# Kernel tuning notes

Hardware: AMD Instinct MI355X
Metric: run time of the kernel (lower is better)

## Reference

```python
import jax, jax.numpy as jnp
import numpy as np


def setup_inputs() -> dict:
    key = jax.random.key(0)
    k1, k2, k3, k4 = jax.random.split(key, 4)
    B, T, C, H = 8, 2048, 1024, 1024
    return {
        "x": jax.random.normal(k1, (B, T, C), dtype=jnp.float32),
        "Wk": jax.random.normal(k2, (H, C), dtype=jnp.float32),
        "Wq": jax.random.normal(k3, (H, C), dtype=jnp.float32),
        "Wv": jax.random.normal(k4, (H, C), dtype=jnp.float32),
    }


def reference(x, Wk, Wq, Wv):
    # x: [B, T, C]; Wk/Wq/Wv: [H, C] (torch Linear stores [fan_out, fan_in])
    B, T, C = x.shape
    k = jnp.einsum('btc,hc->bth', x, Wk)  # [B, T, H]
    q = jnp.einsum('btc,hc->bth', x, Wq)
    v = jnp.einsum('btc,hc->bth', x, Wv)
    # NOTE: source scales by n_embd (C) ** -0.5, not head_size
    wei = jnp.einsum('bth,bsh->bts', q, k) * (C ** -0.5)  # [B, T, T]
    causal = jnp.tril(jnp.ones((T, T), dtype=bool))
    wei = jnp.where(causal, wei, -jnp.inf)
    wei = jax.nn.softmax(wei, axis=-1)
    # Dropout omitted (inference behavior; p=0.5 train-only in source)
    out = jnp.einsum('bts,bsh->bth', wei, v)  # [B, T, H]
    return (out, wei)
```

## Files before the change

### kernel.cpp

```cpp
#include <hip/hip_runtime.h>
#include <hip/hip_bf16.h>


#define BB 8
#define TT 2048
#define CC 1024
#define HH 1024
#define BT (BB * TT)

typedef _Float16 f16x8 __attribute__((ext_vector_type(8)));
typedef _Float16 f16x4 __attribute__((ext_vector_type(4)));
typedef float f32x4 __attribute__((ext_vector_type(4)));

#define AS1 __attribute__((address_space(1)))
#define AS3 __attribute__((address_space(3)))

__device__ __forceinline__ void gld16(const _Float16* g, _Float16* lds) {
    __builtin_amdgcn_global_load_lds((AS1 const unsigned int*)g,
                                     (AS3 unsigned int*)lds, 16, 0, 0);
}

__global__ __launch_bounds__(256) void split_kernel(
    const float* __restrict__ src, _Float16* __restrict__ dh,
    _Float16* __restrict__ dl, int n)
{
    int i = (blockIdx.x * 256 + threadIdx.x) * 4;
    if (i >= n) return;
    float4 v = *(const float4*)(src + i);
    f16x4 h, l;
    h[0] = (_Float16)v.x; l[0] = (_Float16)(v.x - (float)h[0]);
    h[1] = (_Float16)v.y; l[1] = (_Float16)(v.y - (float)h[1]);
    h[2] = (_Float16)v.z; l[2] = (_Float16)(v.z - (float)h[2]);
    h[3] = (_Float16)v.w; l[3] = (_Float16)(v.w - (float)h[3]);
    *(f16x4*)&dh[i] = h;
    *(f16x4*)&dl[i] = l;
}

__global__ __launch_bounds__(256) void splitT_kernel(
    const float* __restrict__ W, _Float16* __restrict__ th,
    _Float16* __restrict__ tl)
{
    __shared__ float L[64][65];
    const int h0 = blockIdx.x * 64;
    const int c0 = blockIdx.y * 64;
    const int tid = threadIdx.x;
    {
        const int hl = tid >> 2;
        const int cs = (tid & 3) * 16;
#pragma unroll
        for (int jj = 0; jj < 16; jj += 4) {
            float4 v = *(const float4*)&W[(size_t)(h0 + hl) * CC + c0 + cs + jj];
            L[cs + jj + 0][hl] = v.x;
            L[cs + jj + 1][hl] = v.y;
            L[cs + jj + 2][hl] = v.z;
            L[cs + jj + 3][hl] = v.w;
        }
    }
    __syncthreads();
    const int c  = tid >> 2;
    const int hs = (tid & 3) * 16;
    f16x8 hv0, hv1, lv0, lv1;
#pragma unroll
    for (int i = 0; i < 8; ++i) {
        float a = L[c][hs + i], b = L[c][hs + 8 + i];
        hv0[i] = (_Float16)a; lv0[i] = (_Float16)(a - (float)hv0[i]);
        hv1[i] = (_Float16)b; lv1[i] = (_Float16)(b - (float)hv1[i]);
    }
    size_t o = (size_t)(c0 + c) * HH + h0 + hs;
    *(f16x8*)&th[o] = hv0; *(f16x8*)&th[o + 8] = hv1;
    *(f16x8*)&tl[o] = lv0; *(f16x8*)&tl[o + 8] = lv1;
}

__global__ __launch_bounds__(256, 2) void mm_kernel(
    const _Float16* __restrict__ aH, const _Float16* __restrict__ aL,
    const _Float16* __restrict__ bH, const _Float16* __restrict__ bL,
    _Float16* __restrict__ mtH, _Float16* __restrict__ mtL)
{
    __shared__ _Float16 Ah[4096], Al[4096], Bh[4096], Bl[4096];

    const int n0 = blockIdx.x * 128;
    const int m0 = blockIdx.y * 128;

    const int tid  = threadIdx.x;
    const int r0   = tid & 127;
    const int k0   = tid >> 7;
    const int wave = tid >> 6;
    const int lane = tid & 63;
    const int quad = lane >> 4;
    const int lrow = lane & 15;
    const int wr   = (wave >> 1) * 64;
    const int wc   = (wave & 1) * 64;

    const size_t ga = (size_t)(m0 + r0) * HH + k0 * 8;
    const size_t gb = (size_t)(n0 + r0) * HH + k0 * 8;
    const int lds0 = tid * 8, lds1 = (tid + 256) * 8;

    f32x4 acc[4][4] = {};

    for (int kc = 0; kc < HH; kc += 32) {
        __syncthreads();
        gld16(aH + ga + kc,      &Ah[lds0]);
        gld16(aH + ga + kc + 16, &Ah[lds1]);
        gld16(aL + ga + kc,      &Al[lds0]);
        gld16(aL + ga + kc + 16, &Al[lds1]);
        gld16(bH + gb + kc,      &Bh[lds0]);
        gld16(bH + gb + kc + 16, &Bh[lds1]);
        gld16(bL + gb + kc,      &Bl[lds0]);
        gld16(bL + gb + kc + 16, &Bl[lds1]);
        __syncthreads();

        f16x8 ahf[4], alf[4], bhf[4], blf[4];
#pragma unroll
        for (int i = 0; i < 4; ++i) {
            ahf[i] = *(const f16x8*)&Ah[(quad * 128 + wr + i * 16 + lrow) * 8];
            alf[i] = *(const f16x8*)&Al[(quad * 128 + wr + i * 16 + lrow) * 8];
            bhf[i] = *(const f16x8*)&Bh[(quad * 128 + wc + i * 16 + lrow) * 8];
            blf[i] = *(const f16x8*)&Bl[(quad * 128 + wc + i * 16 + lrow) * 8];
        }
#pragma unroll
        for (int i = 0; i < 4; ++i)
#pragma unroll
            for (int j = 0; j < 4; ++j) {
                acc[i][j] = __builtin_amdgcn_mfma_f32_16x16x32_f16(ahf[i], bhf[j], acc[i][j], 0, 0, 0);
                acc[i][j] = __builtin_amdgcn_mfma_f32_16x16x32_f16(ahf[i], blf[j], acc[i][j], 0, 0, 0);
                acc[i][j] = __builtin_amdgcn_mfma_f32_16x16x32_f16(alf[i], bhf[j], acc[i][j], 0, 0, 0);
            }
    }

#pragma unroll
    for (int i = 0; i < 4; ++i)
#pragma unroll
        for (int j = 0; j < 4; ++j) {
            int mm = m0 + wr + i * 16 + quad * 4;
            int nn = n0 + wc + j * 16 + lrow;
            f16x4 ph, pl;
#pragma unroll
            for (int r = 0; r < 4; ++r) {
                float val = acc[i][j][r];
                _Float16 h = (_Float16)val;
                ph[r] = h;
                pl[r] = (_Float16)(val - (float)h);
            }
            *(f16x4*)&mtH[(size_t)nn * CC + mm] = ph;
            *(f16x4*)&mtL[(size_t)nn * CC + mm] = pl;
        }
}

#define EPI_STRIDE 136
__global__ __launch_bounds__(256, 2) void pv_kernel(
    const _Float16* __restrict__ xh, const _Float16* __restrict__ xl,
    const _Float16* __restrict__ mtH, const _Float16* __restrict__ mtL,
    const _Float16* __restrict__ Wvh,
    _Float16* __restrict__ Ph, _Float16* __restrict__ Pl,
    _Float16* __restrict__ vT)
{
    __shared__ _Float16 S[40960];

    const int idx   = blockIdx.x;
    const int z     = idx >> 10;
    const int r     = idx & 1023;
    const int xcd   = r & 7;
    const int j7    = r >> 3;
    const int mtile = xcd * 16 + (j7 >> 3);
    const int ntile = j7 & 7;
    const int m0 = mtile * 128;
    const int n0 = ntile * 128;

    const int tid  = threadIdx.x;
    const int r0   = tid & 127;
    const int k0   = tid >> 7;
    const int wave = tid >> 6;
    const int lane = tid & 63;
    const int quad = lane >> 4;
    const int lrow = lane & 15;
    const int wr   = (wave >> 1) * 64;
    const int wc   = (wave & 1) * 64;

    const size_t ga = (size_t)(m0 + r0) * CC + k0 * 8;
    const size_t gb = (size_t)(n0 + r0) * CC + k0 * 8;
    const int lds0 = tid * 8, lds1 = (tid + 256) * 8;

    f32x4 acc[4][4] = {};

    if (z == 0) {
#define PV_A(kc_, sp_) do { \
        _Float16* Sb = S + (sp_) * 8192; \
        gld16(xh + ga + (kc_),      &Sb[lds0]); \
        gld16(xh + ga + (kc_) + 16, &Sb[lds1]); \
        gld16(xl + ga + (kc_),      &Sb[4096 + lds0]); \
        gld16(xl + ga + (kc_) + 16, &Sb[4096 + lds1]); \
    } while (0)
#define PV_B(kc_, sp_) do { \
        _Float16* Sb = S + 24576 + (sp_) * 8192; \
        gld16(mtH + gb + (kc_),      &Sb[lds0]); \
        gld16(mtH + gb + (kc_) + 16, &Sb[lds1]); \
        gld16(mtL + gb + (kc_),      &Sb[4096 + lds0]); \
        gld16(mtL + gb + (kc_) + 16, &Sb[4096 + lds1]); \
    } while (0)
        PV_A(0, 0);
        PV_B(0, 0);
        PV_A(32, 1);
        int sa = 0, sb = 0;
        for (int kc = 0; kc < CC; kc += 32) {
            asm volatile("s_waitcnt vmcnt(4)" ::: "memory");
            __builtin_amdgcn_s_barrier();
            __builtin_amdgcn_sched_barrier(0);

            int kb = kc + 32; if (kb > CC - 32) kb = CC - 32;
            PV_B(kb, sb ^ 1);
            int ka = kc + 64; if (ka > CC - 32) ka = CC - 32;
            int s2 = sa + 2; if (s2 >= 3) s2 -= 3;
            PV_A(ka, s2);

            const _Float16* Ah = S + sa * 8192;
            const _Float16* Al = Ah + 4096;
            const _Float16* Bh = S + 24576 + sb * 8192;
            const _Float16* Bl = Bh + 4096;

            f16x8 ahf[4], alf[4], bhf[4], blf[4];
#pragma unroll
            for (int i = 0; i < 4; ++i) {
                ahf[i] = *(const f16x8*)&Ah[(quad * 128 + wr + i * 16 + lrow) * 8];
                alf[i] = *(const f16x8*)&Al[(quad * 128 + wr + i * 16 + lrow) * 8];
                bhf[i] = *(const f16x8*)&Bh[(quad * 128 + wc + i * 16 + lrow) * 8];
                blf[i] = *(const f16x8*)&Bl[(quad * 128 + wc + i * 16 + lrow) * 8];
            }
#pragma unroll
            for (int i = 0; i < 4; ++i)
#pragma unroll
                for (int j = 0; j < 4; ++j) {
                    acc[i][j] = __builtin_amdgcn_mfma_f32_16x16x32_f16(ahf[i], bhf[j], acc[i][j], 0, 0, 0);
                    acc[i][j] = __builtin_amdgcn_mfma_f32_16x16x32_f16(ahf[i], blf[j], acc[i][j], 0, 0, 0);
                    acc[i][j] = __builtin_amdgcn_mfma_f32_16x16x32_f16(alf[i], bhf[j], acc[i][j], 0, 0, 0);
                }

            ++sa; if (sa == 3) sa = 0;
            sb ^= 1;
        }
    } else {
#define PV_S1(kc_, sp_) do { \
        _Float16* Sb = S + (sp_) * 8192; \
        gld16(xh  + ga + (kc_),      &Sb[lds0]); \
        gld16(xh  + ga + (kc_) + 16, &Sb[lds1]); \
        gld16(Wvh + gb + (kc_),      &Sb[4096 + lds0]); \
        gld16(Wvh + gb + (kc_) + 16, &Sb[4096 + lds1]); \
    } while (0)
        PV_S1(0, 0);
        PV_S1(32, 1);
        int sl = 0;
        for (int kc = 0; kc < CC; kc += 32) {
            asm volatile("s_waitcnt vmcnt(4)" ::: "memory");
            __builtin_amdgcn_s_barrier();
            __builtin_amdgcn_sched_barrier(0);

            int kpre = kc + 64;
            if (kpre > CC - 32) kpre = CC - 32;
            int s2 = sl + 2; if (s2 >= 3) s2 -= 3;
            PV_S1(kpre, s2);

            const _Float16* Ah = S + sl * 8192;
            const _Float16* Bh = Ah + 4096;

            f16x8 ahf[4], bhf[4];
#pragma unroll
            for (int i = 0; i < 4; ++i) {
                ahf[i] = *(const f16x8*)&Ah[(quad * 128 + wr + i * 16 + lrow) * 8];
                bhf[i] = *(const f16x8*)&Bh[(quad * 128 + wc + i * 16 + lrow) * 8];
            }
#pragma unroll
            for (int i = 0; i < 4; ++i)
#pragma unroll
                for (int j = 0; j < 4; ++j)
                    acc[i][j] = __builtin_amdgcn_mfma_f32_16x16x32_f16(ahf[i], bhf[j], acc[i][j], 0, 0, 0);

            ++sl; if (sl == 3) sl = 0;
        }
    }

    asm volatile("s_waitcnt vmcnt(0)" ::: "memory");
    __syncthreads();

    if (z == 1) {
#pragma unroll
        for (int i = 0; i < 4; ++i)
#pragma unroll
            for (int j = 0; j < 4; ++j) {
                int hl = wc + j * 16 + lrow;
                int tl = wr + i * 16 + quad * 4;
                f16x4 p;
#pragma unroll
                for (int rr = 0; rr < 4; ++rr) p[rr] = (_Float16)acc[i][j][rr];
                *(f16x4*)&S[hl * EPI_STRIDE + tl] = p;
            }
        __syncthreads();
        const int bi  = mtile >> 4;
        const int t0g = (mtile & 15) * 128;
        _Float16* vb = vT + (size_t)bi * HH * TT;
#pragma unroll
        for (int rr = 0; rr < 128; rr += 16) {
            int h = rr + (tid >> 4);
            int t = (tid & 15) * 8;
            f16x8 val = *(const f16x8*)&S[h * EPI_STRIDE + t];
            *(f16x8*)&vb[(size_t)(n0 + h) * TT + t0g + t] = val;
        }
    } else {
#pragma unroll
        for (int i = 0; i < 4; ++i)
#pragma unroll
            for (int j = 0; j < 4; ++j) {
                int tl = wr + i * 16 + quad * 4;
                int cl = wc + j * 16 + lrow;
#pragma unroll
                for (int rr = 0; rr < 4; ++rr)
                    S[(tl + rr) * EPI_STRIDE + cl] = (_Float16)acc[i][j][rr];
            }
        __syncthreads();
#pragma unroll
        for (int rr = 0; rr < 128; rr += 16) {
            int t = rr + (tid >> 4);
            int c = (tid & 15) * 8;
            f16x8 val = *(const f16x8*)&S[t * EPI_STRIDE + c];
            *(f16x8*)&Ph[(size_t)(m0 + t) * CC + n0 + c] = val;
        }
        __syncthreads();
#pragma unroll
        for (int i = 0; i < 4; ++i)
#pragma unroll
            for (int j = 0; j < 4; ++j) {
                int tl = wr + i * 16 + quad * 4;
                int cl = wc + j * 16 + lrow;
#pragma unroll
                for (int rr = 0; rr < 4; ++rr) {
                    float val = acc[i][j][rr];
                    _Float16 h = (_Float16)val;
                    S[(tl + rr) * EPI_STRIDE + cl] = (_Float16)(val - (float)h);
                }
            }
        __syncthreads();
#pragma unroll
        for (int rr = 0; rr < 128; rr += 16) {
            int t = rr + (tid >> 4);
            int c = (tid & 15) * 8;
            f16x8 val = *(const f16x8*)&S[t * EPI_STRIDE + c];
            *(f16x8*)&Pl[(size_t)(m0 + t) * CC + n0 + c] = val;
        }
    }
}

__global__ __launch_bounds__(256, 2) void logits_kernel(
    const _Float16* __restrict__ Ph, const _Float16* __restrict__ Pl,
    const _Float16* __restrict__ xh, const _Float16* __restrict__ xl,
    float* __restrict__ wei)
{
    __shared__ _Float16 S[40960];

    const int id  = blockIdx.x;
    const int b   = id & 7;
    const int tri = id >> 3;
    int tt = (int)((sqrtf(8.0f * (float)tri + 1.0f) - 1.0f) * 0.5f);
    while ((tt + 1) * (tt + 2) / 2 <= tri) ++tt;
    while (tt * (tt + 1) / 2 > tri) --tt;
    const int st = tri - tt * (tt + 1) / 2;

    const size_t base = (size_t)b * TT * CC;
    float* wb = wei + (size_t)b * TT * TT;
    const int m0 = tt * 128;
    const int n0 = st * 128;

    const int tid  = threadIdx.x;
    const int r0   = tid & 127;
    const int k0   = tid >> 7;
    const int wave = tid >> 6;
    const int lane = tid & 63;
    const int quad = lane >> 4;
    const int lrow = lane & 15;
    const int wr   = (wave >> 1) * 64;
    const int wc   = (wave & 1) * 64;

    const size_t ga = base + (size_t)(m0 + r0) * CC + k0 * 8;
    const size_t gb = base + (size_t)(n0 + r0) * CC + k0 * 8;
    const int lds0 = tid * 8, lds1 = (tid + 256) * 8;

    f32x4 acc[4][4] = {};

#define LG_A(kc_, sp_) do { \
    _Float16* Sb = S + (sp_) * 8192; \
    gld16(Ph + ga + (kc_),      &Sb[lds0]); \
    gld16(Ph + ga + (kc_) + 16, &Sb[lds1]); \
    gld16(Pl + ga + (kc_),      &Sb[4096 + lds0]); \
    gld16(Pl + ga + (kc_) + 16, &Sb[4096 + lds1]); \
} while (0)
#define LG_B(kc_, sp_) do { \
    _Float16* Sb = S + 24576 + (sp_) * 8192; \
    gld16(xh + gb + (kc_),      &Sb[lds0]); \
    gld16(xh + gb + (kc_) + 16, &Sb[lds1]); \
    gld16(xl + gb + (kc_),      &Sb[4096 + lds0]); \
    gld16(xl + gb + (kc_) + 16, &Sb[4096 + lds1]); \
} while (0)

    LG_A(0, 0);
    LG_B(0, 0);
    LG_A(32, 1);

    int sa = 0, sb = 0;
    for (int kc = 0; kc < CC; kc += 32) {
        asm volatile("s_waitcnt vmcnt(4)" ::: "memory");
        __builtin_amdgcn_s_barrier();
        __builtin_amdgcn_sched_barrier(0);

        int kb = kc + 32; if (kb > CC - 32) kb = CC - 32;
        LG_B(kb, sb ^ 1);
        int ka = kc + 64; if (ka > CC - 32) ka = CC - 32;
        int s2 = sa + 2; if (s2 >= 3) s2 -= 3;
        LG_A(ka, s2);

        const _Float16* Ah = S + sa * 8192;
        const _Float16* Al = Ah + 4096;
        const _Float16* Bh = S + 24576 + sb * 8192;
        const _Float16* Bl = Bh + 4096;

        f16x8 ahf[4], alf[4], bhf[4], blf[4];
#pragma unroll
        for (int i = 0; i < 4; ++i) {
            ahf[i] = *(const f16x8*)&Ah[(quad * 128 + wr + i * 16 + lrow) * 8];
            alf[i] = *(const f16x8*)&Al[(quad * 128 + wr + i * 16 + lrow) * 8];
            bhf[i] = *(const f16x8*)&Bh[(quad * 128 + wc + i * 16 + lrow) * 8];
            blf[i] = *(const f16x8*)&Bl[(quad * 128 + wc + i * 16 + lrow) * 8];
        }
#pragma unroll
        for (int i = 0; i < 4; ++i)
#pragma unroll
            for (int j = 0; j < 4; ++j) {
                acc[i][j] = __builtin_amdgcn_mfma_f32_16x16x32_f16(ahf[i], bhf[j], acc[i][j], 0, 0, 0);
                acc[i][j] = __builtin_amdgcn_mfma_f32_16x16x32_f16(ahf[i], blf[j], acc[i][j], 0, 0, 0);
                acc[i][j] = __builtin_amdgcn_mfma_f32_16x16x32_f16(alf[i], bhf[j], acc[i][j], 0, 0, 0);
            }

        ++sa; if (sa == 3) sa = 0;
        sb ^= 1;
    }

    asm volatile("s_waitcnt vmcnt(0)" ::: "memory");

    const float scale = 0.03125f;
#pragma unroll
    for (int i = 0; i < 4; ++i)
#pragma unroll
        for (int j = 0; j < 4; ++j)
#pragma unroll
            for (int r = 0; r < 4; ++r) {
                int rr = wr + i * 16 + quad * 4 + r;
                int cc = wc + j * 16 + lrow;
                wb[(size_t)(m0 + rr) * TT + n0 + cc] = acc[i][j][r] * scale;
            }
}

__global__ __launch_bounds__(256) void softmax_kernel(
    float* __restrict__ wei, _Float16* __restrict__ wei16)
{
    const int t = blockIdx.x;
    const int b = blockIdx.y;
    float* row = wei + (size_t)b * TT * TT + (size_t)t * TT;
    _Float16* row16 = wei16 + (size_t)b * TT * TT + (size_t)t * TT;
    const int n = t + 1;
    const int tid = threadIdx.x;
    const int base = tid * 8;

    float vals[8];
    if (base < n) {
        float4 v0 = *(const float4*)&row[base];
        float4 v1 = *(const float4*)&row[base + 4];
        vals[0] = v0.x; vals[1] = v0.y; vals[2] = v0.z; vals[3] = v0.w;
        vals[4] = v1.x; vals[5] = v1.y; vals[6] = v1.z; vals[7] = v1.w;
    } else {
#pragma unroll
        for (int i = 0; i < 8; ++i) vals[i] = -INFINITY;
    }

    float mx = -INFINITY;
#pragma unroll
    for (int i = 0; i < 8; ++i) {
        if (base + i >= n) vals[i] = -INFINITY;
        mx = fmaxf(mx, vals[i]);
    }
#pragma unroll
    for (int off = 32; off > 0; off >>= 1)
        mx = fmaxf(mx, __shfl_down(mx, off));

    __shared__ float redm[4];
    __shared__ float reds[4];
    if ((tid & 63) == 0) redm[tid >> 6] = mx;
    __syncthreads();
    const float m = fmaxf(fmaxf(redm[0], redm[1]), fmaxf(redm[2], redm[3]));

    float sum = 0.f;
#pragma unroll
    for (int i = 0; i < 8; ++i) {
        vals[i] = __expf(vals[i] - m);
        sum += vals[i];
    }
#pragma unroll
    for (int off = 32; off > 0; off >>= 1)
        sum += __shfl_down(sum, off);
    if ((tid & 63) == 0) reds[tid >> 6] = sum;
    __syncthreads();
    const float inv = 1.0f / (reds[0] + reds[1] + reds[2] + reds[3]);

    f16x8 h;
#pragma unroll
    for (int i = 0; i < 8; ++i) {
        float w = vals[i] * inv;
        vals[i] = w;
        h[i] = (_Float16)w;
    }
    *(float4*)&row[base]     = make_float4(vals[0], vals[1], vals[2], vals[3]);
    *(float4*)&row[base + 4] = make_float4(vals[4], vals[5], vals[6], vals[7]);
    *(f16x8*)&row16[base]    = h;
}

__global__ __launch_bounds__(256, 3) void out_kernel(
    const _Float16* __restrict__ wei16, const _Float16* __restrict__ vT,
    float* __restrict__ out)
{
    __shared__ _Float16 S[24576];

    const int id = blockIdx.x;
    const int b  = id & 7;
    const int r  = id >> 3;
    const int tt = 15 - (r >> 3);
    const int nb = r & 7;

    const _Float16* wb = wei16 + (size_t)b * TT * TT;
    const _Float16* vb = vT    + (size_t)b * HH * TT;
    float*          ob = out   + (size_t)b * TT * HH;

    const int m0 = tt * 128;
    const int n0 = nb * 128;
    const int kend = (tt + 1) * 128;

    const int tid  = threadIdx.x;
    const int r0   = tid & 127;
    const int k0   = tid >> 7;
    const int wave = tid >> 6;
    const int lane = tid & 63;
    const int quad = lane >> 4;
    const int lrow = lane & 15;
    const int wr   = (wave >> 1) * 64;
    const int wc   = (wave & 1) * 64;

    const size_t ga = (size_t)(m0 + r0) * TT + k0 * 8;
    const size_t gb = (size_t)(n0 + r0) * TT + k0 * 8;
    const int lds0 = tid * 8, lds1 = (tid + 256) * 8;

    f32x4 acc[4][4] = {};

#define OUT_STAGE(kc_, sp_) do { \
    _Float16* Sb = S + (sp_) * 8192; \
    gld16(wb + ga + (kc_),      &Sb[lds0]); \
    gld16(wb + ga + (kc_) + 16, &Sb[lds1]); \
    gld16(vb + gb + (kc_),      &Sb[4096 + lds0]); \
    gld16(vb + gb + (kc_) + 16, &Sb[4096 + lds1]); \
} while (0)

    OUT_STAGE(0, 0);
    OUT_STAGE(32, 1);

    int sl = 0;
    for (int kc = 0; kc < kend; kc += 32) {
        asm volatile("s_waitcnt vmcnt(4)" ::: "memory");
        __builtin_amdgcn_s_barrier();
        __builtin_amdgcn_sched_barrier(0);

        int kpre = kc + 64;
        if (kpre > kend - 32) kpre = kend - 32;
        int s2 = sl + 2; if (s2 >= 3) s2 -= 3;
        OUT_STAGE(kpre, s2);

        const _Float16* Ah = S + sl * 8192;
        const _Float16* Bh = Ah + 4096;

        f16x8 ahf[4], bhf[4];
#pragma unroll
        for (int i = 0; i < 4; ++i) {
            ahf[i] = *(const f16x8*)&Ah[(quad * 128 + wr + i * 16 + lrow) * 8];
            bhf[i] = *(const f16x8*)&Bh[(quad * 128 + wc + i * 16 + lrow) * 8];
        }
#pragma unroll
        for (int i = 0; i < 4; ++i)
#pragma unroll
            for (int j = 0; j < 4; ++j)
                acc[i][j] = __builtin_amdgcn_mfma_f32_16x16x32_f16(ahf[i], bhf[j], acc[i][j], 0, 0, 0);

        ++sl; if (sl == 3) sl = 0;
    }

    asm volatile("s_waitcnt vmcnt(0)" ::: "memory");

#pragma unroll
    for (int i = 0; i < 4; ++i)
#pragma unroll
        for (int j = 0; j < 4; ++j)
#pragma unroll
            for (int r2 = 0; r2 < 4; ++r2) {
                int rr = wr + i * 16 + quad * 4 + r2;
                int cc = wc + j * 16 + lrow;
                ob[(size_t)(m0 + rr) * HH + n0 + cc] = acc[i][j][r2];
            }
}

extern "C" void kernel_launch(void* const* d_in, const int* in_sizes, int n_in,
                              void* d_out, int out_size, void* d_ws, size_t ws_size,
                              hipStream_t stream)
{
    const float* x  = (const float*)d_in[0];
    const float* Wk = (const float*)d_in[1];
    const float* Wq = (const float*)d_in[2];
    const float* Wv = (const float*)d_in[3];

    const size_t NX = (size_t)BT * CC;
    const size_t NW = (size_t)HH * CC;

    float* out = (float*)d_out;
    float* wei = out + (size_t)BT * HH;

    _Float16* WqTh = (_Float16*)out;
    _Float16* WqTl = WqTh + NW;
    _Float16* WkTh = WqTl + NW;
    _Float16* WkTl = WkTh + NW;
    _Float16* Wvh  = WkTl + NW;
    _Float16* Wvl  = Wvh  + NW;
    _Float16* MTh  = Wvl  + NW;
    _Float16* MTl  = MTh  + NW;

    _Float16* xh = (_Float16*)d_ws;
    _Float16* xl = xh + NX;
    _Float16* Ph = xl + NX;
    _Float16* Pl = Ph + NX;
    _Float16* vT = Pl + NX;
    _Float16* wei16 = (_Float16*)d_ws;

    split_kernel<<<dim3(NX / 1024), 256, 0, stream>>>(x, xh, xl, (int)NX);
    splitT_kernel<<<dim3(HH / 64, CC / 64), 256, 0, stream>>>(Wq, WqTh, WqTl);
    splitT_kernel<<<dim3(HH / 64, CC / 64), 256, 0, stream>>>(Wk, WkTh, WkTl);
    split_kernel<<<dim3(NW / 1024), 256, 0, stream>>>(Wv, Wvh, Wvl, (int)NW);

    mm_kernel<<<dim3(CC / 128, CC / 128), 256, 0, stream>>>(
        WqTh, WqTl, WkTh, WkTl, MTh, MTl);
    pv_kernel<<<dim3(2048), 256, 0, stream>>>(
        xh, xl, MTh, MTl, Wvh, Ph, Pl, vT);
    logits_kernel<<<dim3(136 * BB), 256, 0, stream>>>(
        Ph, Pl, xh, xl, wei);
    softmax_kernel<<<dim3(TT, BB), 256, 0, stream>>>(wei, wei16);
    out_kernel<<<dim3(128 * BB), 256, 0, stream>>>(wei16, vT, out);
}
```

Baseline: 797.9 us.

## Enlarge pv and off-diagonal logits tiles to 256x256 with 512-thread blocks

Rewrites pv_kernel and the off-diagonal part of the logits GEMM to use 256x256 output tiles, 512-thread blocks and a simple double-buffered LDS pipeline. Diagonal logits tiles move to a separate kernel that keeps 128x128 tiles. The larger tiles raise arithmetic intensity and cut global/L2 traffic per FLOP. In exchange there is higher register pressure (8x4 accumulators), 128KB of LDS per block, fewer blocks for load balancing, and the older finer-grained vmcnt pipelining is dropped.

Measured after the change: 843.8 us. 1.06x slower.

```diff
diff --git a/kernel.cpp b/kernel.cpp
--- a/kernel.cpp
+++ b/kernel.cpp
@@ -146,25 +146,284 @@
         }
 }
 
-#define EPI_STRIDE 136
-__global__ __launch_bounds__(256, 2) void pv_kernel(
+__global__ __launch_bounds__(512, 2) void pv_kernel(
     const _Float16* __restrict__ xh, const _Float16* __restrict__ xl,
     const _Float16* __restrict__ mtH, const _Float16* __restrict__ mtL,
     const _Float16* __restrict__ Wvh,
     _Float16* __restrict__ Ph, _Float16* __restrict__ Pl,
     _Float16* __restrict__ vT)
 {
+    __shared__ _Float16 S[65536];
+
+    const int id = blockIdx.x;
+    const int z  = id & 1;
+    const int q  = id >> 1;
+    const int xcd = q & 7;
+    const int s   = q >> 3;
+    const int mtile = xcd * 8 + (s >> 2);
+    const int ntile = s & 3;
+    const int m0 = mtile * 256;
+    const int n0 = ntile * 256;
+
+    const int tid  = threadIdx.x;
+    const int wave = tid >> 6;
+    const int lane = tid & 63;
+    const int quad = lane >> 4;
+    const int lrow = lane & 15;
+    const int mw   = wave >> 2;
+    const int nw   = wave & 3;
+
+    const size_t ga = (size_t)(m0 + (tid & 255)) * CC + (tid >> 8) * 8;
+    const size_t gb = (size_t)(n0 + (tid & 255)) * CC + (tid >> 8) * 8;
+    const int lds0 = tid * 8, lds1 = (tid + 512) * 8;
+
+    f32x4 acc[8][4] = {};
+
+    if (z == 0) {
+#define ST0(kc_, buf_) do { \
+        _Float16* Sb = S + (buf_) * 32768; \
+        gld16(xh  + ga + (kc_),      &Sb[lds0]); \
+        gld16(xh  + ga + (kc_) + 16, &Sb[lds1]); \
+        gld16(xl  + ga + (kc_),      &Sb[8192 + lds0]); \
+        gld16(xl  + ga + (kc_) + 16, &Sb[8192 + lds1]); \
+        gld16(mtH + gb + (kc_),      &Sb[16384 + lds0]); \
+        gld16(mtH + gb + (kc_) + 16, &Sb[16384 + lds1]); \
+        gld16(mtL + gb + (kc_),      &Sb[24576 + lds0]); \
+        gld16(mtL + gb + (kc_) + 16, &Sb[24576 + lds1]); \
+    } while (0)
+        ST0(0, 0);
+        int cur = 0;
+        for (int kc = 0; kc < CC; kc += 32) {
+            __syncthreads();
+            if (kc + 32 < CC) ST0(kc + 32, cur ^ 1);
+
+            const _Float16* Ab = S + cur * 32768;
+            const _Float16* Al_ = Ab + 8192;
+            const _Float16* Bb = Ab + 16384;
+            const _Float16* Bl_ = Ab + 24576;
+
+            f16x8 bh[4], bl[4];
+#pragma unroll
+            for (int j = 0; j < 4; ++j) {
+                int c = (quad * 256 + nw * 64 + j * 16 + lrow) * 8;
+                bh[j] = *(const f16x8*)&Bb[c];
+                bl[j] = *(const f16x8*)&Bl_[c];
+            }
+#pragma unroll
+            for (int i = 0; i < 8; ++i) {
+                int a = (quad * 256 + mw * 128 + i * 16 + lrow) * 8;
+                f16x8 ah = *(const f16x8*)&Ab[a];
+                f16x8 al = *(const f16x8*)&Al_[a];
+#pragma unroll
+                for (int j = 0; j < 4; ++j) {
+                    acc[i][j] = __builtin_amdgcn_mfma_f32_16x16x32_f16(ah, bh[j], acc[i][j], 0, 0, 0);
+                    acc[i][j] = __builtin_amdgcn_mfma_f32_16x16x32_f16(ah, bl[j], acc[i][j], 0, 0, 0);
+                    acc[i][j] = __builtin_amdgcn_mfma_f32_16x16x32_f16(al, bh[j], acc[i][j], 0, 0, 0);
+                }
+            }
+            cur ^= 1;
+        }
+
+#pragma unroll
+        for (int stream = 0; stream < 2; ++stream) {
+            _Float16* dst = stream ? Pl : Ph;
+#pragma unroll
+            for (int h = 0; h < 2; ++h) {
+                __syncthreads();
+                if (mw == h) {
+#pragma unroll
+                    for (int i = 0; i < 8; ++i)
+#pragma unroll
+                        for (int j = 0; j < 4; ++j)
+#pragma unroll
+                            for (int rr = 0; rr < 4; ++rr) {
+                                float v = acc[i][j][rr];
+                                _Float16 hi = (_Float16)v;
+                                _Float16 e = stream ? (_Float16)(v - (float)hi) : hi;
+                                S[(i * 16 + quad * 4 + rr) * 264 + nw * 64 + j * 16 + lrow] = e;
+                            }
+                }
+                __syncthreads();
+#pragma unroll
+                for (int w = 0; w < 8; ++w) {
+                    int x = w * 512 + tid;
+                    int row = x >> 5;
+                    int c8 = (x & 31) * 8;
+                    *(f16x8*)&dst[(size_t)(m0 + h * 128 + row) * CC + n0 + c8] =
+                        *(const f16x8*)&S[row * 264 + c8];
+                }
+            }
+        }
+    } else {
+#define ST1(kc_, buf_) do { \
+        _Float16* Sb = S + (buf_) * 16384; \
+        gld16(xh  + ga + (kc_),      &Sb[lds0]); \
+        gld16(xh  + ga + (kc_) + 16, &Sb[lds1]); \
+        gld16(Wvh + gb + (kc_),      &Sb[8192 + lds0]); \
+        gld16(Wvh + gb + (kc_) + 16, &Sb[8192 + lds1]); \
+    } while (0)
+        ST1(0, 0);
+        int cur = 0;
+        for (int kc = 0; kc < CC; kc += 32) {
+            __syncthreads();
+            if (kc + 32 < CC) ST1(kc + 32, cur ^ 1);
+
+            const _Float16* Ab = S + cur * 16384;
+            const _Float16* Bb = Ab + 8192;
+
+            f16x8 bh[4];
+#pragma unroll
+            for (int j = 0; j < 4; ++j)
+                bh[j] = *(const f16x8*)&Bb[(quad * 256 + nw * 64 + j * 16 + lrow) * 8];
+#pragma unroll
+            for (int i = 0; i < 8; ++i) {
+                f16x8 ah = *(const f16x8*)&Ab[(quad * 256 + mw * 128 + i * 16 + lrow) * 8];
+#pragma unroll
+                for (int j = 0; j < 4; ++j)
+                    acc[i][j] = __builtin_amdgcn_mfma_f32_16x16x32_f16(ah, bh[j], acc[i][j], 0, 0, 0);
+            }
+            cur ^= 1;
+        }
+
+        const int bi  = mtile >> 3;
+        const int t0g = (mtile & 7) * 256;
+        _Float16* vb = vT + (size_t)bi * HH * TT;
+#pragma unroll
+        for (int h = 0; h < 2; ++h) {
+            __syncthreads();
+            if (mw == h) {
+#pragma unroll
+                for (int i = 0; i < 8; ++i)
+#pragma unroll
+                    for (int j = 0; j < 4; ++j) {
+                        f16x4 p;
+#pragma unroll
+                        for (int rr = 0; rr < 4; ++rr) p[rr] = (_Float16)acc[i][j][rr];
+                        *(f16x4*)&S[(nw * 64 + j * 16 + lrow) * 136 + i * 16 + quad * 4] = p;
+                    }
+            }
+            __syncthreads();
+#pragma unroll
+            for (int w = 0; w < 8; ++w) {
+                int x = w * 512 + tid;
+                int hrow = x >> 4;
+                int t8 = (x & 15) * 8;
+                *(f16x8*)&vb[(size_t)(n0 + hrow) * TT + t0g + h * 128 + t8] =
+                    *(const f16x8*)&S[hrow * 136 + t8];
+            }
+        }
+    }
+}
+
+__global__ __launch_bounds__(512, 2) void logits_kernel(
+    const _Float16* __restrict__ Ph, const _Float16* __restrict__ Pl,
+    const _Float16* __restrict__ xh, const _Float16* __restrict__ xl,
+    float* __restrict__ wei)
+{
+    __shared__ _Float16 S[65536];
+
+    const int id = blockIdx.x;
+    const int b  = id & 7;
+    const int q  = id >> 3;
+    int tt = 1; while (tt * (tt + 1) / 2 <= q) ++tt;
+    const int st = q - tt * (tt - 1) / 2;
+
+    const size_t base = (size_t)b * TT * CC;
+    float* wb = wei + (size_t)b * TT * TT;
+    const int m0 = tt * 256;
+    const int n0 = st * 256;
+
+    const int tid  = threadIdx.x;
+    const int wave = tid >> 6;
+    const int lane = tid & 63;
+    const int quad = lane >> 4;
+    const int lrow = lane & 15;
+    const int mw   = wave >> 2;
+    const int nw   = wave & 3;
+
+    const size_t ga = base + (size_t)(m0 + (tid & 255)) * CC + (tid >> 8) * 8;
+    const size_t gb = base + (size_t)(n0 + (tid & 255)) * CC + (tid >> 8) * 8;
+    const int lds0 = tid * 8, lds1 = (tid + 512) * 8;
+
+    f32x4 acc[8][4] = {};
+
+#define STL(kc_, buf_) do { \
+    _Float16* Sb = S + (buf_) * 32768; \
+    gld16(Ph + ga + (kc_),      &Sb[lds0]); \
+    gld16(Ph + ga + (kc_) + 16, &Sb[lds1]); \
+    gld16(Pl + ga + (kc_),      &Sb[8192 + lds0]); \
+    gld16(Pl + ga + (kc_) + 16, &Sb[8192 + lds1]); \
+    gld16(xh + gb + (kc_),      &Sb[16384 + lds0]); \
+    gld16(xh + gb + (kc_) + 16, &Sb[16384 + lds1]); \
+    gld16(xl + gb + (kc_),      &Sb[24576 + lds0]); \
+    gld16(xl + gb + (kc_) + 16, &Sb[24576 + lds1]); \
+} while (0)
+
+    STL(0, 0);
+    int cur = 0;
+    for (int kc = 0; kc < CC; kc += 32) {
+        __syncthreads();
+        if (kc + 32 < CC) STL(kc + 32, cur ^ 1);
+
+        const _Float16* Ab = S + cur * 32768;
+        const _Float16* Al_ = Ab + 8192;
+        const _Float16* Bb = Ab + 16384;
+        const _Float16* Bl_ = Ab + 24576;
+
+        f16x8 bh[4], bl[4];
+#pragma unroll
+        for (int j = 0; j < 4; ++j) {
+            int c = (quad * 256 + nw * 64 + j * 16 + lrow) * 8;
+            bh[j] = *(const f16x8*)&Bb[c];
+            bl[j] = *(const f16x8*)&Bl_[c];
+        }
+#pragma unroll
+        for (int i = 0; i < 8; ++i) {
+            int a = (quad * 256 + mw * 128 + i * 16 + lrow) * 8;
+            f16x8 ah = *(const f16x8*)&Ab[a];
+            f16x8 al = *(const f16x8*)&Al_[a];
+#pragma unroll
+            for (int j = 0; j < 4; ++j) {
+                acc[i][j] = __builtin_amdgcn_mfma_f32_16x16x32_f16(ah, bh[j], acc[i][j], 0, 0, 0);
+                acc[i][j] = __builtin_amdgcn_mfma_f32_16x16x32_f16(ah, bl[j], acc[i][j], 0, 0, 0);
+                acc[i][j] = __builtin_amdgcn_mfma_f32_16x16x32_f16(al, bh[j], acc[i][j], 0, 0, 0);
+            }
+        }
+        cur ^= 1;
+    }
+
+    const float scale = 0.03125f;
+#pragma unroll
+    for (int i = 0; i < 8; ++i)
+#pragma unroll
+        for (int j = 0; j < 4; ++j)
+#pragma unroll
+            for (int r = 0; r < 4; ++r) {
+                int rr = mw * 128 + i * 16 + quad * 4 + r;
+                int cc = nw * 64 + j * 16 + lrow;
+                wb[(size_t)(m0 + rr) * TT + n0 + cc] = acc[i][j][r] * scale;
+            }
+}
+
+__global__ __launch_bounds__(256, 2) void logits_diag_kernel(
+    const _Float16* __restrict__ Ph, const _Float16* __restrict__ Pl,
+    const _Float16* __restrict__ xh, const _Float16* __restrict__ xl,
+    float* __restrict__ wei)
+{
     __shared__ _Float16 S[40960];
 
-    const int idx   = blockIdx.x;
-    const int z     = idx >> 10;
-    const int r     = idx & 1023;
-    const int xcd   = r & 7;
-    const int j7    = r >> 3;
-    const int mtile = xcd * 16 + (j7 >> 3);
-    const int ntile = j7 & 7;
-    const int m0 = mtile * 128;
-    const int n0 = ntile * 128;
+    const int id = blockIdx.x;
+    const int b  = id & 7;
+    const int qq = id >> 3;
+    const int d  = qq / 3;
+    const int rm = qq - d * 3;
+    const int tt = 2 * d + (rm > 0 ? 1 : 0);
+    const int st = 2 * d + (rm == 2 ? 1 : 0);
+
+    const size_t base = (size_t)b * TT * CC;
+    float* wb = wei + (size_t)b * TT * TT;
+    const int m0 = tt * 128;
+    const int n0 = st * 128;
 
     const int tid  = threadIdx.x;
     const int r0   = tid & 127;
@@ -176,196 +435,166 @@
     const int wr   = (wave >> 1) * 64;
     const int wc   = (wave & 1) * 64;
 
-    const size_t ga = (size_t)(m0 + r0) * CC + k0 * 8;
-    const size_t gb = (size_t)(n0 + r0) * CC + k0 * 8;
+    const size_t ga = base + (size_t)(m0 + r0) * CC + k0 * 8;
+    const size_t gb = base + (size_t)(n0 + r0) * CC + k0 * 8;
     const int lds0 = tid * 8, lds1 = (tid + 256) * 8;
 
     f32x4 acc[4][4] = {};
 
-    if (z == 0) {
-#define PV_A(kc_, sp_) do { \
-        _Float16* Sb = S + (sp_) * 8192; \
-        gld16(xh + ga + (kc_),      &Sb[lds0]); \
-        gld16(xh + ga + (kc_) + 16, &Sb[lds1]); \
-        gld16(xl + ga + (kc_),      &Sb[4096 + lds0]); \
-        gld16(xl + ga + (kc_) + 16, &Sb[4096 + lds1]); \
-    } while (0)
-#define PV_B(kc_, sp_) do { \
-        _Float16* Sb = S + 24576 + (sp_) * 8192; \
-        gld16(mtH + gb + (kc_),      &Sb[lds0]); \
-        gld16(mtH + gb + (kc_) + 16, &Sb[lds1]); \
-        gld16(mtL + gb + (kc_),      &Sb[4096 + lds0]); \
-        gld16(mtL + gb + (kc_) + 16, &Sb[4096 + lds1]); \
-    } while (0)
-        PV_A(0, 0);
-        PV_B(0, 0);
-        PV_A(32, 1);
-        int sa = 0, sb = 0;
-        for (int kc = 0; kc < CC; kc += 32) {
-            asm volatile("s_waitcnt vmcnt(4)" ::: "memory");
-            __builtin_amdgcn_s_barrier();
-            __builtin_amdgcn_sched_barrier(0);
-
-            int kb = kc + 32; if (kb > CC - 32) kb = CC - 32;
-            PV_B(kb, sb ^ 1);
-            int ka = kc + 64; if (ka > CC - 32) ka = CC - 32;
-            int s2 = sa + 2; if (s2 >= 3) s2 -= 3;
-            PV_A(ka, s2);
-
-            const _Float16* Ah = S + sa * 8192;
-            const _Float16* Al = Ah + 4096;
-            const _Float16* Bh = S + 24576 + sb * 8192;
-            const _Float16* Bl = Bh + 4096;
-
-            f16x8 ahf[4], alf[4], bhf[4], blf[4];
-#pragma unroll
-            for (int i = 0; i < 4; ++i) {
-                ahf[i] = *(const f16x8*)&Ah[(quad * 128 + wr + i * 16 + lrow) * 8];
-                alf[i] = *(const f16x8*)&Al[(quad * 128 + wr + i * 16 + lrow) * 8];
-                bhf[i] = *(const f16x8*)&Bh[(quad * 128 + wc + i * 16 + lrow) * 8];
-                blf[i] = *(const f16x8*)&Bl[(quad * 128 + wc + i * 16 + lrow) * 8];
-            }
-#pragma unroll
-            for (int i = 0; i < 4; ++i)
-#pragma unroll
-                for (int j = 0; j < 4; ++j) {
-                    acc[i][j] = __builtin_amdgcn_mfma_f32_16x16x32_f16(ahf[i], bhf[j], acc[i][j], 0, 0, 0);
-                    acc[i][j] = __builtin_amdgcn_mfma_f32_16x16x32_f16(ahf[i], blf[j], acc[i][j], 0, 0, 0);
-                    acc[i][j] = __builtin_amdgcn_mfma_f32_16x16x32_f16(alf[i], bhf[j], acc[i][j], 0, 0, 0);
-                }
-
-            ++sa; if (sa == 3) sa = 0;
-            sb ^= 1;
-        }
+#define DG_A(kc_, sp_) do { \
+    _Float16* Sb = S + (sp_) * 8192; \
+    gld16(Ph + ga + (kc_),      &Sb[lds0]); \
+    gld16(Ph + ga + (kc_) + 16, &Sb[lds1]); \
+    gld16(Pl + ga + (kc_),      &Sb[4096 + lds0]); \
+    gld16(Pl + ga + (kc_) + 16, &Sb[4096 + lds1]); \
+} while (0)
+#define DG_B(kc_, sp_) do { \
+    _Float16* Sb = S + 24576 + (sp_) * 8192; \
+    gld16(xh + gb + (kc_),      &Sb[lds0]); \
+    gld16(xh + gb + (kc_) + 16, &Sb[lds1]); \
+    gld16(xl + gb + (kc_),      &Sb[4096 + lds0]); \
+    gld16(xl + gb + (kc_) + 16, &Sb[4096 + lds1]); \
+} while (0)
+
+    DG_A(0, 0);
+    DG_B(0, 0);
+    DG_A(32, 1);
+
+    int sa = 0, sb = 0;
+    for (int kc = 0; kc < CC; kc += 32) {
+        asm volatile("s_waitcnt vmcnt(4)" ::: "memory");
+        __builtin_amdgcn_s_barrier();
+        __builtin_amdgcn_sched_barrier(0);
+
+        int kb = kc + 32; if (kb > CC - 32) kb = CC - 32;
+        DG_B(kb, sb ^ 1);
+        int ka = kc + 64; if (ka > CC - 32) ka = CC - 32;
+        int s2 = sa + 2; if (s2 >= 3) s2 -= 3;
+        DG_A(ka, s2);
+
+        const _Float16* Ah = S + sa * 8192;
+        const _Float16* Al = Ah + 4096;
+        const _Float16* Bh = S + 24576 + sb * 8192;
+        const _Float16* Bl = Bh + 4096;
+
+        f16x8 ahf[4], alf[4], bhf[4], blf[4];
+#pragma unroll
+        for (int i = 0; i < 4; ++i) {
+            ahf[i] = *(const f16x8*)&Ah[(quad * 128 + wr + i * 16 + lrow) * 8];
+            alf[i] = *(const f16x8*)&Al[(quad * 128 + wr + i * 16 + lrow) * 8];
+            bhf[i] = *(const f16x8*)&Bh[(quad * 128 + wc + i * 16 + lrow) * 8];
+            blf[i] = *(const f16x8*)&Bl[(quad * 128 + wc + i * 16 + lrow) * 8];
+        }
+#pragma unroll
+        for (int i = 0; i < 4; ++i)
+#pragma unroll
+            for (int j = 0; j < 4; ++j) {
+                acc[i][j] = __builtin_amdgcn_mfma_f32_16x16x32_f16(ahf[i], bhf[j], acc[i][j], 0, 0, 0);
+                acc[i][j] = __builtin_amdgcn_mfma_f32_16x16x32_f16(ahf[i], blf[j], acc[i][j], 0, 0, 0);
+                acc[i][j] = __builtin_amdgcn_mfma_f32_16x16x32_f16(alf[i], bhf[j], acc[i][j], 0, 0, 0);
+            }
+
+        ++sa; if (sa == 3) sa = 0;
+        sb ^= 1;
+    }
+
+    asm volatile("s_waitcnt vmcnt(0)" ::: "memory");
+
+    const float scale = 0.03125f;
+#pragma unroll
+    for (int i = 0; i < 4; ++i)
+#pragma unroll
+        for (int j = 0; j < 4; ++j)
+#pragma unroll
+            for (int r = 0; r < 4; ++r) {
+                int rr = wr + i * 16 + quad * 4 + r;
+                int cc = wc + j * 16 + lrow;
+                wb[(size_t)(m0 + rr) * TT + n0 + cc] = acc[i][j][r] * scale;
+            }
+}
+
+__global__ __launch_bounds__(256) void softmax_kernel(
+    float* __restrict__ wei, _Float16* __restrict__ wei16)
+{
+    const int t = blockIdx.x;
+    const int b = blockIdx.y;
+    float* row = wei + (size_t)b * TT * TT + (size_t)t * TT;
+    _Float16* row16 = wei16 + (size_t)b * TT * TT + (size_t)t * TT;
+    const int n = t + 1;
+    const int tid = threadIdx.x;
+    const int base = tid * 8;
+
+    float vals[8];
+    if (base < n) {
+        float4 v0 = *(const float4*)&row[base];
+        float4 v1 = *(const float4*)&row[base + 4];
+        vals[0] = v0.x; vals[1] = v0.y; vals[2] = v0.z; vals[3] = v0.w;
+        vals[4] = v1.x; vals[5] = v1.y; vals[6] = v1.z; vals[7] = v1.w;
     } else {
-#define PV_S1(kc_, sp_) do { \
-        _Float16* Sb = S + (sp_) * 8192; \
-        gld16(xh  + ga + (kc_),      &Sb[lds0]); \
-        gld16(xh  + ga + (kc_) + 16, &Sb[lds1]); \
-        gld16(Wvh + gb + (kc_),      &Sb[4096 + lds0]); \
-        gld16(Wvh + gb + (kc_) + 16, &Sb[4096 + lds1]); \
-    } while (0)
-        PV_S1(0, 0);
-        PV_S1(32, 1);
-        int sl = 0;
-        for (int kc = 0; kc < CC; kc += 32) {
-            asm volatile("s_waitcnt vmcnt(4)" ::: "memory");
-            __builtin_amdgcn_s_barrier();
-            __builtin_amdgcn_sched_barrier(0);
-
-            int kpre = kc + 64;
-            if (kpre > CC - 32) kpre = CC - 32;
-            int s2 = sl + 2; if (s2 >= 3) s2 -= 3;
-            PV_S1(kpre, s2);
-
-            const _Float16* Ah = S + sl * 8192;
-            const _Float16* Bh = Ah + 4096;
-
-            f16x8 ahf[4], bhf[4];
-#pragma unroll
-            for (int i = 0; i < 4; ++i) {
-                ahf[i] = *(const f16x8*)&Ah[(quad * 128 + wr + i * 16 + lrow) * 8];
-                bhf[i] = *(const f16x8*)&Bh[(quad * 128 + wc + i * 16 + lrow) * 8];
-            }
-#pragma unroll
-            for (int i = 0; i < 4; ++i)
-#pragma unroll
-                for (int j = 0; j < 4; ++j)
-                    acc[i][j] = __builtin_amdgcn_mfma_f32_16x16x32_f16(ahf[i], bhf[j], acc[i][j], 0, 0, 0);
-
-            ++sl; if (sl == 3) sl = 0;
-        }
-    }
-
-    asm volatile("s_waitcnt vmcnt(0)" ::: "memory");
+#pragma unroll
+        for (int i = 0; i < 8; ++i) vals[i] = -INFINITY;
+    }
+
+    float mx = -INFINITY;
+#pragma unroll
+    for (int i = 0; i < 8; ++i) {
+        if (base + i >= n) vals[i] = -INFINITY;
+        mx = fmaxf(mx, vals[i]);
+    }
+#pragma unroll
+    for (int off = 32; off > 0; off >>= 1)
+        mx = fmaxf(mx, __shfl_down(mx, off));
+
+    __shared__ float redm[4];
+    __shared__ float reds[4];
+    if ((tid & 63) == 0) redm[tid >> 6] = mx;
     __syncthreads();
-
-    if (z == 1) {
-#pragma unroll
-        for (int i = 0; i < 4; ++i)
-#pragma unroll
-            for (int j = 0; j < 4; ++j) {
-                int hl = wc + j * 16 + lrow;
-                int tl = wr + i * 16 + quad * 4;
-                f16x4 p;
-#pragma unroll
-                for (int rr = 0; rr < 4; ++rr) p[rr] = (_Float16)acc[i][j][rr];
-                *(f16x4*)&S[hl * EPI_STRIDE + tl] = p;
-            }
-        __syncthreads();
-        const int bi  = mtile >> 4;
-        const int t0g = (mtile & 15) * 128;
-        _Float16* vb = vT + (size_t)bi * HH * TT;
-#pragma unroll
-        for (int rr = 0; rr < 128; rr += 16) {
-            int h = rr + (tid >> 4);
-            int t = (tid & 15) * 8;
-            f16x8 val = *(const f16x8*)&S[h * EPI_STRIDE + t];
-            *(f16x8*)&vb[(size_t)(n0 + h) * TT + t0g + t] = val;
-        }
-    } else {
-#pragma unroll
-        for (int i = 0; i < 4; ++i)
-#pragma unroll
-            for (int j = 0; j < 4; ++j) {
-                int tl = wr + i * 16 + quad * 4;
-                int cl = wc + j * 16 + lrow;
-#pragma unroll
-                for (int rr = 0; rr < 4; ++rr)
-                    S[(tl + rr) * EPI_STRIDE + cl] = (_Float16)acc[i][j][rr];
-            }
-        __syncthreads();
-#pragma unroll
-        for (int rr = 0; rr < 128; rr += 16) {
-            int t = rr + (tid >> 4);
-            int c = (tid & 15) * 8;
-            f16x8 val = *(const f16x8*)&S[t * EPI_STRIDE + c];
-            *(f16x8*)&Ph[(size_t)(m0 + t) * CC + n0 + c] = val;
-        }
-        __syncthreads();
-#pragma unroll
-        for (int i = 0; i < 4; ++i)
-#pragma unroll
-            for (int j = 0; j < 4; ++j) {
-                int tl = wr + i * 16 + quad * 4;
-                int cl = wc + j * 16 + lrow;
-#pragma unroll
-                for (int rr = 0; rr < 4; ++rr) {
-                    float val = acc[i][j][rr];
-                    _Float16 h = (_Float16)val;
-                    S[(tl + rr) * EPI_STRIDE + cl] = (_Float16)(val - (float)h);
-                }
-            }
-        __syncthreads();
-#pragma unroll
-        for (int rr = 0; rr < 128; rr += 16) {
-            int t = rr + (tid >> 4);
-            int c = (tid & 15) * 8;
-            f16x8 val = *(const f16x8*)&S[t * EPI_STRIDE + c];
-            *(f16x8*)&Pl[(size_t)(m0 + t) * CC + n0 + c] = val;
-        }
-    }
-}
-
-__global__ __launch_bounds__(256, 2) void logits_kernel(
-    const _Float16* __restrict__ Ph, const _Float16* __restrict__ Pl,
-    const _Float16* __restrict__ xh, const _Float16* __restrict__ xl,
-    float* __restrict__ wei)
-{
-    __shared__ _Float16 S[40960];
-
-    const int id  = blockIdx.x;
-    const int b   = id & 7;
-    const int tri = id >> 3;
-    int tt = (int)((sqrtf(8.0f * (float)tri + 1.0f) - 1.0f) * 0.5f);
-    while ((tt + 1) * (tt + 2) / 2 <= tri) ++tt;
-    while (tt * (tt + 1) / 2 > tri) --tt;
-    const int st = tri - tt * (tt + 1) / 2;
-
-    const size_t base = (size_t)b * TT * CC;
-    float* wb = wei + (size_t)b * TT * TT;
+    const float m = fmaxf(fmaxf(redm[0], redm[1]), fmaxf(redm[2], redm[3]));
+
+    float sum = 0.f;
+#pragma unroll
+    for (int i = 0; i < 8; ++i) {
+        vals[i] = __expf(vals[i] - m);
+        sum += vals[i];
+    }
+#pragma unroll
+    for (int off = 32; off > 0; off >>= 1)
+        sum += __shfl_down(sum, off);
+    if ((tid & 63) == 0) reds[tid >> 6] = sum;
+    __syncthreads();
+    const float inv = 1.0f / (reds[0] + reds[1] + reds[2] + reds[3]);
+
+    f16x8 h;
+#pragma unroll
+    for (int i = 0; i < 8; ++i) {
+        float w = vals[i] * inv;
+        vals[i] = w;
+        h[i] = (_Float16)w;
+    }
+    *(float4*)&row[base]     = make_float4(vals[0], vals[1], vals[2], vals[3]);
+    *(float4*)&row[base + 4] = make_float4(vals[4], vals[5], vals[6], vals[7]);
+    *(f16x8*)&row16[base]    = h;
+}
+
+__global__ __launch_bounds__(256, 3) void out_kernel(
+    const _Float16* __restrict__ wei16, const _Float16* __restrict__ vT,
+    float* __restrict__ out)
+{
+    __shared__ _Float16 S[24576];
+
+    const int id = blockIdx.x;
+    const int b  = id & 7;
+    const int r  = id >> 3;
+    const int tt = 15 - (r >> 3);
+    const int nb = r & 7;
+
+    const _Float16* wb = wei16 + (size_t)b * TT * TT;
+    const _Float16* vb = vT    + (size_t)b * HH * TT;
+    float*          ob = out   + (size_t)b * TT * HH;
+
     const int m0 = tt * 128;
-    const int n0 = st * 128;
+    const int n0 = nb * 128;
+    const int kend = (tt + 1) * 128;
 
     const int tid  = threadIdx.x;
     const int r0   = tid & 127;
@@ -377,177 +606,6 @@
     const int wr   = (wave >> 1) * 64;
     const int wc   = (wave & 1) * 64;
 
-    const size_t ga = base + (size_t)(m0 + r0) * CC + k0 * 8;
-    const size_t gb = base + (size_t)(n0 + r0) * CC + k0 * 8;
-    const int lds0 = tid * 8, lds1 = (tid + 256) * 8;
-
-    f32x4 acc[4][4] = {};
-
-#define LG_A(kc_, sp_) do { \
-    _Float16* Sb = S + (sp_) * 8192; \
-    gld16(Ph + ga + (kc_),      &Sb[lds0]); \
-    gld16(Ph + ga + (kc_) + 16, &Sb[lds1]); \
-    gld16(Pl + ga + (kc_),      &Sb[4096 + lds0]); \
-    gld16(Pl + ga + (kc_) + 16, &Sb[4096 + lds1]); \
-} while (0)
-#define LG_B(kc_, sp_) do { \
-    _Float16* Sb = S + 24576 + (sp_) * 8192; \
-    gld16(xh + gb + (kc_),      &Sb[lds0]); \
-    gld16(xh + gb + (kc_) + 16, &Sb[lds1]); \
-    gld16(xl + gb + (kc_),      &Sb[4096 + lds0]); \
-    gld16(xl + gb + (kc_) + 16, &Sb[4096 + lds1]); \
-} while (0)
-
-    LG_A(0, 0);
-    LG_B(0, 0);
-    LG_A(32, 1);
-
-    int sa = 0, sb = 0;
-    for (int kc = 0; kc < CC; kc += 32) {
-        asm volatile("s_waitcnt vmcnt(4)" ::: "memory");
-        __builtin_amdgcn_s_barrier();
-        __builtin_amdgcn_sched_barrier(0);
-
-        int kb = kc + 32; if (kb > CC - 32) kb = CC - 32;
-        LG_B(kb, sb ^ 1);
-        int ka = kc + 64; if (ka > CC - 32) ka = CC - 32;
-        int s2 = sa + 2; if (s2 >= 3) s2 -= 3;
-        LG_A(ka, s2);
-
-        const _Float16* Ah = S + sa * 8192;
-        const _Float16* Al = Ah + 4096;
-        const _Float16* Bh = S + 24576 + sb * 8192;
-        const _Float16* Bl = Bh + 4096;
-
-        f16x8 ahf[4], alf[4], bhf[4], blf[4];
-#pragma unroll
-        for (int i = 0; i < 4; ++i) {
-            ahf[i] = *(const f16x8*)&Ah[(quad * 128 + wr + i * 16 + lrow) * 8];
-            alf[i] = *(const f16x8*)&Al[(quad * 128 + wr + i * 16 + lrow) * 8];
-            bhf[i] = *(const f16x8*)&Bh[(quad * 128 + wc + i * 16 + lrow) * 8];
-            blf[i] = *(const f16x8*)&Bl[(quad * 128 + wc + i * 16 + lrow) * 8];
-        }
-#pragma unroll
-        for (int i = 0; i < 4; ++i)
-#pragma unroll
-            for (int j = 0; j < 4; ++j) {
-                acc[i][j] = __builtin_amdgcn_mfma_f32_16x16x32_f16(ahf[i], bhf[j], acc[i][j], 0, 0, 0);
-                acc[i][j] = __builtin_amdgcn_mfma_f32_16x16x32_f16(ahf[i], blf[j], acc[i][j], 0, 0, 0);
-                acc[i][j] = __builtin_amdgcn_mfma_f32_16x16x32_f16(alf[i], bhf[j], acc[i][j], 0, 0, 0);
-            }
-
-        ++sa; if (sa == 3) sa = 0;
-        sb ^= 1;
-    }
-
-    asm volatile("s_waitcnt vmcnt(0)" ::: "memory");
-
-    const float scale = 0.03125f;
-#pragma unroll
-    for (int i = 0; i < 4; ++i)
-#pragma unroll
-        for (int j = 0; j < 4; ++j)
-#pragma unroll
-            for (int r = 0; r < 4; ++r) {
-                int rr = wr + i * 16 + quad * 4 + r;
-                int cc = wc + j * 16 + lrow;
-                wb[(size_t)(m0 + rr) * TT + n0 + cc] = acc[i][j][r] * scale;
-            }
-}
-
-__global__ __launch_bounds__(256) void softmax_kernel(
-    float* __restrict__ wei, _Float16* __restrict__ wei16)
-{
-    const int t = blockIdx.x;
-    const int b = blockIdx.y;
-    float* row = wei + (size_t)b * TT * TT + (size_t)t * TT;
-    _Float16* row16 = wei16 + (size_t)b * TT * TT + (size_t)t * TT;
-    const int n = t + 1;
-    const int tid = threadIdx.x;
-    const int base = tid * 8;
-
-    float vals[8];
-    if (base < n) {
-        float4 v0 = *(const float4*)&row[base];
-        float4 v1 = *(const float4*)&row[base + 4];
-        vals[0] = v0.x; vals[1] = v0.y; vals[2] = v0.z; vals[3] = v0.w;
-        vals[4] = v1.x; vals[5] = v1.y; vals[6] = v1.z; vals[7] = v1.w;
-    } else {
-#pragma unroll
-        for (int i = 0; i < 8; ++i) vals[i] = -INFINITY;
-    }
-
-    float mx = -INFINITY;
-#pragma unroll
-    for (int i = 0; i < 8; ++i) {
-        if (base + i >= n) vals[i] = -INFINITY;
-        mx = fmaxf(mx, vals[i]);
-    }
-#pragma unroll
-    for (int off = 32; off > 0; off >>= 1)
-        mx = fmaxf(mx, __shfl_down(mx, off));
-
-    __shared__ float redm[4];
-    __shared__ float reds[4];
-    if ((tid & 63) == 0) redm[tid >> 6] = mx;
-    __syncthreads();
-    const float m = fmaxf(fmaxf(redm[0], redm[1]), fmaxf(redm[2], redm[3]));
-
-    float sum = 0.f;
-#pragma unroll
-    for (int i = 0; i < 8; ++i) {
-        vals[i] = __expf(vals[i] - m);
-        sum += vals[i];
-    }
-#pragma unroll
-    for (int off = 32; off > 0; off >>= 1)
-        sum += __shfl_down(sum, off);
-    if ((tid & 63) == 0) reds[tid >> 6] = sum;
-    __syncthreads();
-    const float inv = 1.0f / (reds[0] + reds[1] + reds[2] + reds[3]);
-
-    f16x8 h;
-#pragma unroll
-    for (int i = 0; i < 8; ++i) {
-        float w = vals[i] * inv;
-        vals[i] = w;
-        h[i] = (_Float16)w;
-    }
-    *(float4*)&row[base]     = make_float4(vals[0], vals[1], vals[2], vals[3]);
-    *(float4*)&row[base + 4] = make_float4(vals[4], vals[5], vals[6], vals[7]);
-    *(f16x8*)&row16[base]    = h;
-}
-
-__global__ __launch_bounds__(256, 3) void out_kernel(
-    const _Float16* __restrict__ wei16, const _Float16* __restrict__ vT,
-    float* __restrict__ out)
-{
-    __shared__ _Float16 S[24576];
-
-    const int id = blockIdx.x;
-    const int b  = id & 7;
-    const int r  = id >> 3;
-    const int tt = 15 - (r >> 3);
-    const int nb = r & 7;
-
-    const _Float16* wb = wei16 + (size_t)b * TT * TT;
-    const _Float16* vb = vT    + (size_t)b * HH * TT;
-    float*          ob = out   + (size_t)b * TT * HH;
-
-    const int m0 = tt * 128;
-    const int n0 = nb * 128;
-    const int kend = (tt + 1) * 128;
-
-    const int tid  = threadIdx.x;
-    const int r0   = tid & 127;
-    const int k0   = tid >> 7;
-    const int wave = tid >> 6;
-    const int lane = tid & 63;
-    const int quad = lane >> 4;
-    const int lrow = lane & 15;
-    const int wr   = (wave >> 1) * 64;
-    const int wc   = (wave & 1) * 64;
-
     const size_t ga = (size_t)(m0 + r0) * TT + k0 * 8;
     const size_t gb = (size_t)(n0 + r0) * TT + k0 * 8;
     const int lds0 = tid * 8, lds1 = (tid + 256) * 8;
@@ -646,9 +704,11 @@
 
     mm_kernel<<<dim3(CC / 128, CC / 128), 256, 0, stream>>>(
         WqTh, WqTl, WkTh, WkTl, MTh, MTl);
-    pv_kernel<<<dim3(2048), 256, 0, stream>>>(
+    pv_kernel<<<dim3(512), 512, 0, stream>>>(
         xh, xl, MTh, MTl, Wvh, Ph, Pl, vT);
-    logits_kernel<<<dim3(136 * BB), 256, 0, stream>>>(
+    logits_kernel<<<dim3(28 * BB), 512, 0, stream>>>(
+        Ph, Pl, xh, xl, wei);
+    logits_diag_kernel<<<dim3(24 * BB), 256, 0, stream>>>(
         Ph, Pl, xh, xl, wei);
     softmax_kernel<<<dim3(TT, BB), 256, 0, stream>>>(wei, wei16);
     out_kernel<<<dim3(128 * BB), 256, 0, stream>>>(wei16, vT, out);
```
